# Optimization experiments

Measured on AMD Instinct MI355X. Metric: run time of the kernel, lower is better.

## Reference

```python
import jax, jax.numpy as jnp
import numpy as np


def _conv(x, w, b):
    # NCHW conv with 'same' padding derived from kernel size (matches nn.Conv2d padding=k//2)
    ph, pw = w.shape[2] // 2, w.shape[3] // 2
    y = jax.lax.conv_general_dilated(
        x, w, window_strides=(1, 1), padding=[(ph, ph), (pw, pw)],
        dimension_numbers=("NCHW", "OIHW", "NCHW"))
    return y + b[None, :, None, None]


def _attn(q, k, v):
    # q,k,v: [N,C,H,W]; spatial self-attention over S=H*W positions
    N, C, H, W = q.shape
    S = H * W
    qf = q.reshape(N, C, S)
    kf = k.reshape(N, C, S)
    vf = v.reshape(N, C, S)
    scores = jnp.einsum("ncs,nct->nst", qf, kf) / jnp.sqrt(jnp.asarray(C, qf.dtype))
    a = jax.nn.softmax(scores, axis=-1)
    z = jnp.einsum("nst,nct->ncs", a, vf)
    return z.reshape(N, C, H, W)


def setup_inputs() -> dict:
    key = jax.random.key(0)
    ks = jax.random.split(key, 14)
    B, T, Ci, Hd, H, W = 4, 10, 1, 64, 32, 32
    sc = 0.05
    return {
        "x": jax.random.uniform(ks[0], (B, T, Ci, H, W), jnp.float32),
        # SAConvLSTMCell main conv: (Ci+Hd) -> 4*Hd, 3x3
        "w_conv": jax.random.normal(ks[1], (4 * Hd, Ci + Hd, 3, 3), jnp.float32) * sc,
        "b_conv": jax.random.normal(ks[2], (4 * Hd,), jnp.float32) * sc,
        # SA conv_h: Hd -> 3*Hd, 1x1
        "w_h": jax.random.normal(ks[3], (3 * Hd, Hd, 1, 1), jnp.float32) * sc,
        "b_h": jax.random.normal(ks[4], (3 * Hd,), jnp.float32) * sc,
        # SA conv_m: Hd -> 2*Hd, 1x1
        "w_m": jax.random.normal(ks[5], (2 * Hd, Hd, 1, 1), jnp.float32) * sc,
        "b_m": jax.random.normal(ks[6], (2 * Hd,), jnp.float32) * sc,
        # SA conv_z: 2*Hd -> Hd, 1x1
        "w_z": jax.random.normal(ks[7], (Hd, 2 * Hd, 1, 1), jnp.float32) * sc,
        "b_z": jax.random.normal(ks[8], (Hd,), jnp.float32) * sc,
        # SA conv_output: 2*Hd -> 3*Hd, 3x3
        "w_sa": jax.random.normal(ks[9], (3 * Hd, 2 * Hd, 3, 3), jnp.float32) * sc,
        "b_sa": jax.random.normal(ks[10], (3 * Hd,), jnp.float32) * sc,
        # conv_out: Hd -> Ci, 1x1
        "w_co": jax.random.normal(ks[11], (Ci, Hd, 1, 1), jnp.float32) * sc,
        "b_co": jax.random.normal(ks[12], (Ci,), jnp.float32) * sc,
        "future_frames": 10,
    }


def reference(x, w_conv, b_conv, w_h, b_h, w_m, b_m, w_z, b_z,
              w_sa, b_sa, w_co, b_co, future_frames):
    B, T, Ci, H, W = x.shape
    Hd = w_conv.shape[0] // 4

    def cell(xt, h, c, m):
        cc = _conv(jnp.concatenate([xt, h], axis=1), w_conv, b_conv)
        i, f, o, g = jnp.split(cc, 4, axis=1)
        c_new = jax.nn.sigmoid(f) * c + jax.nn.sigmoid(i) * jnp.tanh(g)
        h_cur = jax.nn.sigmoid(o) * jnp.tanh(c_new)
        # spatial self-attention memory update
        hq, hk, hv = jnp.split(_conv(h_cur, w_h, b_h), 3, axis=1)
        mk, mv = jnp.split(_conv(m, w_m, b_m), 2, axis=1)
        Zh = _attn(hq, hk, hv)
        Zm = _attn(hq, mk, mv)
        Z = _conv(jnp.concatenate([Zh, Zm], axis=1), w_z, b_z)
        i2, g2, o2 = jnp.split(_conv(jnp.concatenate([Z, h_cur], axis=1), w_sa, b_sa), 3, axis=1)
        i2 = jax.nn.sigmoid(i2)
        m_new = i2 * jnp.tanh(g2) + (1.0 - i2) * m
        h_new = jax.nn.sigmoid(o2) * m_new
        return h_new, c_new, m_new

    z = jnp.zeros((B, Hd, H, W), x.dtype)
    state0 = (z, z, z)

    def enc_step(carry, xt):
        h, c, m = carry
        return cell(xt, h, c, m), None

    (h, c, m), _ = jax.lax.scan(enc_step, state0, jnp.moveaxis(x, 1, 0))

    # first decoder input: raw conv_out(h) (no sigmoid, per the original code path)
    inp0 = _conv(h, w_co, b_co)

    def dec_step(carry, _):
        h, c, m, inp = carry
        h, c, m = cell(inp, h, c, m)
        pred = jax.nn.sigmoid(_conv(h, w_co, b_co))
        return (h, c, m, pred), pred

    _, preds = jax.lax.scan(dec_step, (h, c, m, inp0), None, length=future_frames)
    return jnp.moveaxis(preds, 0, 1)  # [B, future_frames, Ci, H, W]
```

## Files before the change

kernel.cpp:

```cpp
#include <hip/hip_runtime.h>
#include <math.h>

#define SS 1024

typedef unsigned short u16;
typedef __attribute__((ext_vector_type(8))) __bf16 bf16x8;
typedef __attribute__((ext_vector_type(4))) float f32x4;

#define MFMA(a,b,c) __builtin_amdgcn_mfma_f32_16x16x32_bf16(a,b,c,0,0,0)

__device__ __forceinline__ float sigm(float x){ return 1.f/(1.f+__expf(-x)); }
__device__ __forceinline__ u16 f2b(float x){ return __builtin_bit_cast(u16,(__bf16)x); }
__device__ __forceinline__ float b2f(u16 u){ return (float)__builtin_bit_cast(__bf16,u); }
__device__ __forceinline__ bf16x8 ldb8(const u16* p){ return *(const bf16x8*)p; }
__device__ __forceinline__ void st4b(u16* p, const f32x4 v){
  union { u16 u[4]; uint2 w; } t;
  t.u[0]=f2b(v[0]); t.u[1]=f2b(v[1]); t.u[2]=f2b(v[2]); t.u[3]=f2b(v[3]);
  *(uint2*)p = t.w;
}

__global__ __launch_bounds__(256) void k_prep(
    const float* __restrict__ wconv, const float* __restrict__ wh,
    const float* __restrict__ wm, const float* __restrict__ wz,
    const float* __restrict__ wsa,
    u16* __restrict__ Wg, u16* __restrict__ Whm,
    u16* __restrict__ Wzp, u16* __restrict__ Wsap)
{
  const int idx = blockIdx.x*256 + threadIdx.x;
  if (idx < 155648) {
    const int step = idx >> 13, co = (idx >> 5) & 255, j = idx & 31;
    float v = 0.f;
    if (step < 18) {
      const int tap = step >> 1, ci = 1 + (step & 1)*32 + j;
      v = wconv[co*585 + ci*9 + tap];
    } else if (j < 9) {
      v = wconv[co*585 + j];
    }
    Wg[idx] = f2b(v);
    return;
  }
  int l = idx - 155648;
  if (l < 20480) {
    const int step = l / 10240, row = (l >> 5) % 320, j = l & 31;
    const int ci = step*32 + j;
    const float v = (row < 192) ? wh[row*64+ci]*(row < 64 ? 0.125f : 1.f)
                                : wm[(row-192)*64+ci];
    Whm[l] = f2b(v);
    return;
  }
  l -= 20480;
  if (l < 8192) {
    const int step = l >> 11, co = (l >> 5) & 63, j = l & 31;
    Wzp[l] = f2b(wz[co*128 + step*32 + j]);
    return;
  }
  l -= 8192;
  if (l < 221184) {
    const int step = l / 6144, co = (l >> 5) % 192, j = l & 31;
    const int tap = step >> 2, ci = (step & 3)*32 + j;
    Wsap[l] = f2b(wsa[(co*128+ci)*9 + tap]);
  }
}

__global__ __launch_bounds__(512) void k_A(
    const u16* __restrict__ hTb, const float* __restrict__ xsrc, int xbs,
    const u16* __restrict__ Wg, const float* __restrict__ bconv,
    float* __restrict__ cT, u16* __restrict__ xcat,
    const u16* __restrict__ mTb, const u16* __restrict__ Whm,
    const float* __restrict__ bh, const float* __restrict__ bm,
    u16* __restrict__ qT, u16* __restrict__ kT, u16* __restrict__ mkT,
    u16* __restrict__ vC, u16* __restrict__ mvC)
{
  __shared__ u16 hcl[16][72];
  __shared__ float part[4][4][64][4];
  const int b = blockIdx.y, s0 = blockIdx.x*16;
  const int tid = threadIdx.x, wid = tid>>6, lane = tid&63, gl = lane>>4, n = lane&15;
  const int ww = wid & 3, kh = wid >> 2;
  const u16* hb = hTb + (size_t)b*SS*64;
  const int s = s0 + n, y = s>>5, xx = s&31;
  f32x4 acc[4];
#pragma unroll
  for (int g4 = 0; g4 < 4; ++g4) {
    if (kh == 0) {
      const int co = g4*64 + ww*16 + gl*4;
      acc[g4] = (f32x4){ bconv[co], bconv[co+1], bconv[co+2], bconv[co+3] };
    } else {
      acc[g4] = (f32x4){0.f,0.f,0.f,0.f};
    }
  }
#pragma unroll
  for (int ss = 0; ss < 9; ++ss) {
    const int step = kh*9 + ss;
    const int tap = step>>1, half = step&1;
    const int dy = tap/3 - 1, dx = tap%3 - 1;
    const bool ok = ((unsigned)(y+dy) < 32u) & ((unsigned)(xx+dx) < 32u);
    const int sc = ok ? (s + dy*32 + dx) : s;
    bf16x8 bv = ldb8(hb + (size_t)sc*64 + half*32 + gl*8);
    bv = ok ? bv : (bf16x8){};
#pragma unroll
    for (int g4 = 0; g4 < 4; ++g4) {
      const bf16x8 a = ldb8(Wg + step*8192 + (g4*64 + ww*16 + n)*32 + gl*8);
      acc[g4] = MFMA(a, bv, acc[g4]);
    }
  }
  if (kh == 1) {
    bf16x8 xb;
    {
      union { u16 u[8]; bf16x8 v; } t;
#pragma unroll
      for (int jj = 0; jj < 8; ++jj) t.u[jj] = 0;
      if (gl == 0) {
#pragma unroll
        for (int jj = 0; jj < 8; ++jj) {
          const int dy = jj/3 - 1, dx = jj%3 - 1;
          if ((unsigned)(y+dy) < 32u && (unsigned)(xx+dx) < 32u)
            t.u[jj] = f2b(xsrc[b*xbs + s + dy*32 + dx]);
        }
      } else if (gl == 1) {
        if (y+1 < 32 && xx+1 < 32) t.u[0] = f2b(xsrc[b*xbs + s + 33]);
      }
      xb = t.v;
    }
#pragma unroll
    for (int g4 = 0; g4 < 4; ++g4) {
      const bf16x8 a = ldb8(Wg + 18*8192 + (g4*64 + ww*16 + n)*32 + gl*8);
      acc[g4] = MFMA(a, xb, acc[g4]);
    }
#pragma unroll
    for (int g4 = 0; g4 < 4; ++g4)
      *(f32x4*)&part[ww][g4][lane][0] = acc[g4];
  }
  __syncthreads();
  const int r0 = ww*16, cb = r0 + gl*4;
  if (kh == 0) {
#pragma unroll
    for (int g4 = 0; g4 < 4; ++g4) {
      const f32x4 p = *(const f32x4*)&part[ww][g4][lane][0];
      acc[g4][0]+=p[0]; acc[g4][1]+=p[1]; acc[g4][2]+=p[2]; acc[g4][3]+=p[3];
    }
    const int hd0 = cb;
    float* cp = cT + ((size_t)b*SS + s)*64 + hd0;
    f32x4 cv = *(f32x4*)cp, hcv;
#pragma unroll
    for (int rr = 0; rr < 4; ++rr) {
      const float cn = sigm(acc[1][rr])*cv[rr] + sigm(acc[0][rr])*tanhf(acc[3][rr]);
      cv[rr] = cn;
      hcv[rr] = sigm(acc[2][rr])*tanhf(cn);
    }
    *(f32x4*)cp = cv;
    st4b(xcat + ((size_t)b*SS + s)*128 + 64 + hd0, hcv);
    st4b(&hcl[n][hd0], hcv);
  } else {
    f32x4 a3 = (f32x4){ bm[cb], bm[cb+1], bm[cb+2], bm[cb+3] };
    f32x4 a4 = (f32x4){ bm[64+cb], bm[64+cb+1], bm[64+cb+2], bm[64+cb+3] };
#pragma unroll
    for (int step = 0; step < 2; ++step) {
      const bf16x8 bmm = ldb8(mTb + ((size_t)b*SS+s)*64 + step*32 + gl*8);
      a3 = MFMA(ldb8(Whm + step*10240 + (3*64 + r0 + n)*32 + gl*8), bmm, a3);
      a4 = MFMA(ldb8(Whm + step*10240 + (4*64 + r0 + n)*32 + gl*8), bmm, a4);
    }
    const size_t ps = ((size_t)b*SS + s)*64 + cb;
    st4b(mkT + ps, a3);
#pragma unroll
    for (int rr = 0; rr < 4; ++rr)
      mvC[((size_t)b*64 + cb + rr)*SS + s] = f2b(a4[rr]);
  }
  __syncthreads();
  if (kh == 0) {
    f32x4 a0 = (f32x4){ bh[cb]*0.125f, bh[cb+1]*0.125f, bh[cb+2]*0.125f, bh[cb+3]*0.125f };
    f32x4 a1 = (f32x4){ bh[64+cb], bh[64+cb+1], bh[64+cb+2], bh[64+cb+3] };
    f32x4 a2 = (f32x4){ bh[128+cb], bh[128+cb+1], bh[128+cb+2], bh[128+cb+3] };
#pragma unroll
    for (int step = 0; step < 2; ++step) {
      const bf16x8 bhc = ldb8(&hcl[n][step*32 + gl*8]);
      a0 = MFMA(ldb8(Whm + step*10240 + (0*64 + r0 + n)*32 + gl*8), bhc, a0);
      a1 = MFMA(ldb8(Whm + step*10240 + (1*64 + r0 + n)*32 + gl*8), bhc, a1);
      a2 = MFMA(ldb8(Whm + step*10240 + (2*64 + r0 + n)*32 + gl*8), bhc, a2);
    }
    const size_t ps = ((size_t)b*SS + s)*64 + cb;
    st4b(qT + ps, a0);
    st4b(kT + ps, a1);
#pragma unroll
    for (int rr = 0; rr < 4; ++rr)
      vC[((size_t)b*64 + cb + rr)*SS + s] = f2b(a2[rr]);
  }
}

__global__ __launch_bounds__(512) void k_B(
    const u16* __restrict__ qT, const u16* __restrict__ kT,
    const u16* __restrict__ mkT, const u16* __restrict__ vC,
    const u16* __restrict__ mvC,
    const u16* __restrict__ Wzp, const float* __restrict__ bz,
    u16* __restrict__ xcat)
{
  __shared__ u16 ldsP[8*16*72];
  __shared__ float oS[2][3][16][65];
  __shared__ float mS[2][3][16], lS[2][3][16];
  __shared__ u16 zbuf[16][136];
  const int tid = threadIdx.x, wid = tid>>6, lane = tid&63, gl = lane>>4, n = lane&15;
  const int b = blockIdx.y, s0 = blockIdx.x*16;
  const int at = wid & 1, kv = wid >> 1;
  const u16* qb = qT + (size_t)b*SS*64;
  const u16* kb = (at ? mkT : kT) + (size_t)b*SS*64;
  const u16* vb = (at ? mvC : vC) + (size_t)b*64*SS;
  const bf16x8 bq0 = ldb8(qb + (size_t)(s0+n)*64 + gl*8);
  const bf16x8 bq1 = ldb8(qb + (size_t)(s0+n)*64 + 32 + gl*8);
  f32x4 o[4];
#pragma unroll
  for (int ct = 0; ct < 4; ++ct) o[ct] = (f32x4){0.f,0.f,0.f,0.f};
  float mrun = -1e30f, lrun = 0.f;
  u16* pb = ldsP + wid*1152 + n*72;

#pragma unroll 1
  for (int step = 0; step < 4; ++step) {
    const int t0 = kv*256 + step*64;
    f32x4 st4[4];
#pragma unroll
    for (int tt = 0; tt < 4; ++tt) {
      const u16* kr = kb + (size_t)(t0 + tt*16 + n)*64;
      f32x4 a = {0.f,0.f,0.f,0.f};
      a = MFMA(ldb8(kr + gl*8), bq0, a);
      a = MFMA(ldb8(kr + 32 + gl*8), bq1, a);
      st4[tt] = a;
    }
    float mt = -1e30f;
#pragma unroll
    for (int tt = 0; tt < 4; ++tt)
#pragma unroll
      for (int rr = 0; rr < 4; ++rr) mt = fmaxf(mt, st4[tt][rr]);
    mt = fmaxf(mt, __shfl_xor(mt, 16));
    mt = fmaxf(mt, __shfl_xor(mt, 32));
    const float mnew = fmaxf(mrun, mt);
    const float f = __expf(mrun - mnew);
    float ps = 0.f;
#pragma unroll
    for (int tt = 0; tt < 4; ++tt) {
      const float p0e = __expf(st4[tt][0]-mnew), p1e = __expf(st4[tt][1]-mnew);
      const float p2e = __expf(st4[tt][2]-mnew), p3e = __expf(st4[tt][3]-mnew);
      ps += (p0e + p1e) + (p2e + p3e);
      *(unsigned*)(pb + tt*16 + gl*4)     = (unsigned)f2b(p0e) | ((unsigned)f2b(p1e)<<16);
      *(unsigned*)(pb + tt*16 + gl*4 + 2) = (unsigned)f2b(p2e) | ((unsigned)f2b(p3e)<<16);
    }
    ps += __shfl_xor(ps, 16);
    ps += __shfl_xor(ps, 32);
    lrun = lrun*f + ps;
    mrun = mnew;
    float fr[4];
#pragma unroll
    for (int rr = 0; rr < 4; ++rr) fr[rr] = __shfl(f, gl*4 + rr);
#pragma unroll
    for (int ct = 0; ct < 4; ++ct)
#pragma unroll
      for (int rr = 0; rr < 4; ++rr) o[ct][rr] *= fr[rr];
    const bf16x8 pa0 = ldb8(pb + gl*8);
    const bf16x8 pa1 = ldb8(pb + 32 + gl*8);
#pragma unroll
    for (int ct = 0; ct < 4; ++ct) {
      const u16* vr = vb + (size_t)(ct*16 + n)*SS + t0;
      o[ct] = MFMA(pa0, ldb8(vr + gl*8), o[ct]);
      o[ct] = MFMA(pa1, ldb8(vr + 32 + gl*8), o[ct]);
    }
  }
  if (kv > 0) {
#pragma unroll
    for (int ct = 0; ct < 4; ++ct)
#pragma unroll
      for (int rr = 0; rr < 4; ++rr) oS[at][kv-1][gl*4+rr][ct*16+n] = o[ct][rr];
    if (gl == 0) { mS[at][kv-1][n] = mrun; lS[at][kv-1][n] = lrun; }
  }
  __syncthreads();
  if (kv == 0) {
    const float m1 = mS[at][0][n], m2 = mS[at][1][n], m3 = mS[at][2][n];
    const float l1 = lS[at][0][n], l2 = lS[at][1][n], l3 = lS[at][2][n];
    const float mm = fmaxf(fmaxf(mrun, m1), fmaxf(m2, m3));
    const float e0 = __expf(mrun - mm), e1 = __expf(m1 - mm);
    const float e2 = __expf(m2 - mm),   e3 = __expf(m3 - mm);
    const float inv = 1.f / (lrun*e0 + l1*e1 + l2*e2 + l3*e3);
    const float a0 = e0*inv, a1v = e1*inv, a2v = e2*inv, a3v = e3*inv;
    float f0r[4], f1r[4], f2r[4], f3r[4];
#pragma unroll
    for (int rr = 0; rr < 4; ++rr) {
      f0r[rr] = __shfl(a0, gl*4 + rr);
      f1r[rr] = __shfl(a1v, gl*4 + rr);
      f2r[rr] = __shfl(a2v, gl*4 + rr);
      f3r[rr] = __shfl(a3v, gl*4 + rr);
    }
#pragma unroll
    for (int ct = 0; ct < 4; ++ct)
#pragma unroll
      for (int rr = 0; rr < 4; ++rr) {
        const int q = gl*4 + rr, c = ct*16 + n;
        zbuf[q][at*64 + c] = f2b(o[ct][rr]*f0r[rr] + oS[at][0][q][c]*f1r[rr]
                                 + oS[at][1][q][c]*f2r[rr] + oS[at][2][q][c]*f3r[rr]);
      }
  }
  __syncthreads();
  if (wid < 4) {
    const int co = wid*16 + gl*4;
    f32x4 acc = (f32x4){ bz[co], bz[co+1], bz[co+2], bz[co+3] };
#pragma unroll
    for (int qq = 0; qq < 4; ++qq) {
      const bf16x8 bv = ldb8(&zbuf[n][qq*32 + gl*8]);
      const bf16x8 a = ldb8(Wzp + qq*2048 + (wid*16 + n)*32 + gl*8);
      acc = MFMA(a, bv, acc);
    }
    st4b(xcat + ((size_t)b*SS + s0 + n)*128 + co, acc);
  }
}

__global__ __launch_bounds__(768) void k_C(
    const u16* __restrict__ xcat, const u16* __restrict__ Wsap,
    const float* __restrict__ bsa,
    float* __restrict__ mT, u16* __restrict__ mTb, u16* __restrict__ hTb,
    const float* __restrict__ wco, const float* __restrict__ bco,
    float* __restrict__ inp, float* __restrict__ out, int mode, int j)
{
  __shared__ float part[2][4][3][64][4];
  __shared__ float pool[16][17];
  const int b = blockIdx.y, s0 = blockIdx.x*16;
  const int tid = threadIdx.x, wid = tid>>6, lane = tid&63, gl = lane>>4, n = lane&15;
  const int whd = wid & 3, kq = wid >> 2;
  const int hd0 = whd*16 + gl*4;
  const int s = s0 + n, y = s>>5, xx = s&31;
  f32x4 acc[3];
#pragma unroll
  for (int i = 0; i < 3; ++i) {
    if (kq == 0) {
      const int co = i*64 + hd0;
      acc[i] = (f32x4){ bsa[co], bsa[co+1], bsa[co+2], bsa[co+3] };
    } else {
      acc[i] = (f32x4){0.f,0.f,0.f,0.f};
    }
  }
#pragma unroll
  for (int ss = 0; ss < 12; ++ss) {
    const int step = kq*12 + ss;
    const int tap = step>>2, qq = step&3;
    const int dy = tap/3 - 1, dx = tap%3 - 1;
    const bool ok = ((unsigned)(y+dy) < 32u) & ((unsigned)(xx+dx) < 32u);
    const int sc = ok ? (s + dy*32 + dx) : s;
    bf16x8 bv = ldb8(xcat + ((size_t)b*SS + sc)*128 + qq*32 + gl*8);
    bv = ok ? bv : (bf16x8){};
#pragma unroll
    for (int i = 0; i < 3; ++i) {
      const bf16x8 a = ldb8(Wsap + step*6144 + (i*64 + whd*16 + n)*32 + gl*8);
      acc[i] = MFMA(a, bv, acc[i]);
    }
  }
  if (kq > 0) {
#pragma unroll
    for (int i = 0; i < 3; ++i)
      *(f32x4*)&part[kq-1][whd][i][lane][0] = acc[i];
  }
  __syncthreads();
  if (kq == 0) {
#pragma unroll
    for (int i = 0; i < 3; ++i) {
      const f32x4 p0 = *(const f32x4*)&part[0][whd][i][lane][0];
      const f32x4 p1 = *(const f32x4*)&part[1][whd][i][lane][0];
      acc[i][0] += p0[0] + p1[0]; acc[i][1] += p0[1] + p1[1];
      acc[i][2] += p0[2] + p1[2]; acc[i][3] += p0[3] + p1[3];
    }
    float* mp = mT + ((size_t)b*SS + s)*64 + hd0;
    f32x4 mv4 = *(f32x4*)mp, hv;
#pragma unroll
    for (int rr = 0; rr < 4; ++rr) {
      const float i2 = sigm(acc[0][rr]);
      const float mn = i2*tanhf(acc[1][rr]) + (1.f - i2)*mv4[rr];
      mv4[rr] = mn;
      hv[rr] = sigm(acc[2][rr])*mn;
    }
    *(f32x4*)mp = mv4;
    st4b(mTb + ((size_t)b*SS + s)*64 + hd0, mv4);
    st4b(hTb + ((size_t)b*SS + s)*64 + hd0, hv);
    if (mode >= 0)
      pool[n][whd*4 + gl] = hv[0]*wco[hd0] + hv[1]*wco[hd0+1]
                          + hv[2]*wco[hd0+2] + hv[3]*wco[hd0+3];
  }
  if (mode >= 0) {
    __syncthreads();
    if (tid < 16) {
      float v = bco[0];
#pragma unroll
      for (int i = 0; i < 16; ++i) v += pool[tid][i];
      const int sp = s0 + tid;
      if (mode == 1) {
        v = sigm(v);
        out[((size_t)b*10 + j)*SS + sp] = v;
      }
      inp[b*SS + sp] = v;
    }
  }
}

extern "C" void kernel_launch(void* const* d_in, const int* in_sizes, int n_in,
                              void* d_out, int out_size, void* d_ws, size_t ws_size,
                              hipStream_t stream) {
  const float* x      = (const float*)d_in[0];
  const float* w_conv = (const float*)d_in[1];
  const float* b_conv = (const float*)d_in[2];
  const float* w_h    = (const float*)d_in[3];
  const float* b_h    = (const float*)d_in[4];
  const float* w_m    = (const float*)d_in[5];
  const float* b_m    = (const float*)d_in[6];
  const float* w_z    = (const float*)d_in[7];
  const float* b_z    = (const float*)d_in[8];
  const float* w_sa   = (const float*)d_in[9];
  const float* b_sa   = (const float*)d_in[10];
  const float* w_co   = (const float*)d_in[11];
  const float* b_co   = (const float*)d_in[12];
  float* out = (float*)d_out;

  float* ws  = (float*)d_ws;
  float* cT  = ws;
  float* mT  = ws + 262144;
  float* inp = ws + 524288;
  u16* ub   = (u16*)(ws + 528384);
  u16* hTb  = ub;
  u16* mTb  = ub + 262144;
  u16* xcat = ub + 524288;
  u16* qT   = ub + 1048576;
  u16* kT   = ub + 1310720;
  u16* mkT  = ub + 1572864;
  u16* vC   = ub + 1835008;
  u16* mvC  = ub + 2097152;
  u16* Wg   = ub + 2359296;
  u16* Whm  = ub + 2514944;
  u16* Wzp  = ub + 2535424;
  u16* Wsap = ub + 2543616;

  hipMemsetAsync(ws, 0, (size_t)524288*4, stream);
  hipMemsetAsync(hTb, 0, (size_t)524288*2, stream);
  k_prep<<<dim3(1584), 256, 0, stream>>>(w_conv, w_h, w_m, w_z, w_sa, Wg, Whm, Wzp, Wsap);

  auto cell = [&](const float* xsrc, int xbs, int mode, int j) {
    k_A<<<dim3(64,4), 512, 0, stream>>>(hTb, xsrc, xbs, Wg, b_conv, cT, xcat,
                                        mTb, Whm, b_h, b_m, qT, kT, mkT, vC, mvC);
    k_B<<<dim3(64,4), 512, 0, stream>>>(qT, kT, mkT, vC, mvC, Wzp, b_z, xcat);
    k_C<<<dim3(64,4), 768, 0, stream>>>(xcat, Wsap, b_sa, mT, mTb, hTb,
                                        w_co, b_co, inp, out, mode, j);
  };

  for (int t = 0; t < 10; ++t)
    cell(x + (size_t)t*SS, 10*SS, (t == 9) ? 0 : -1, 0);
  for (int j = 0; j < 10; ++j)
    cell(inp, SS, 1, j);
}
```

Baseline: 980.8 us.

## Fold state zeroing into prep kernel, stage x halo in LDS, double-buffer attention P

Drops the two memset launches and zeroes the c, m, h and m-bf16 state buffers inside the weight-prep kernel, which saves launch overhead. In k_A the 3x18 input halo is loaded once into shared memory, so the im2col gather of x reads LDS instead of issuing scattered global loads per lane; this adds one extra __syncthreads. In k_B the softmax P buffer is double-buffered across steps and the step loop is fully unrolled, aiming to remove a write-after-read hazard and allow overlap. In exchange k_B uses more shared memory, which may lower occupancy.

```diff
diff --git a/kernel.cpp b/kernel.cpp
--- a/kernel.cpp
+++ b/kernel.cpp
@@ -24,9 +24,14 @@
     const float* __restrict__ wm, const float* __restrict__ wz,
     const float* __restrict__ wsa,
     u16* __restrict__ Wg, u16* __restrict__ Whm,
-    u16* __restrict__ Wzp, u16* __restrict__ Wsap)
+    u16* __restrict__ Wzp, u16* __restrict__ Wsap,
+    float* __restrict__ cT, float* __restrict__ mT,
+    u16* __restrict__ hTb, u16* __restrict__ mTb)
 {
   const int idx = blockIdx.x*256 + threadIdx.x;
+  if (idx < 262144) {
+    cT[idx] = 0.f; mT[idx] = 0.f; hTb[idx] = 0; mTb[idx] = 0;
+  }
   if (idx < 155648) {
     const int step = idx >> 13, co = (idx >> 5) & 255, j = idx & 31;
     float v = 0.f;
@@ -73,11 +78,21 @@
 {
   __shared__ u16 hcl[16][72];
   __shared__ float part[4][4][64][4];
+  __shared__ float xtile[3][20];
   const int b = blockIdx.y, s0 = blockIdx.x*16;
   const int tid = threadIdx.x, wid = tid>>6, lane = tid&63, gl = lane>>4, n = lane&15;
   const int ww = wid & 3, kh = wid >> 2;
   const u16* hb = hTb + (size_t)b*SS*64;
   const int s = s0 + n, y = s>>5, xx = s&31;
+  if (tid < 60) {
+    const int r = tid/20, c = tid%20;
+    const int yy = (s0>>5) + r - 1, xc = (s0&31) + c - 1;
+    float v = 0.f;
+    if ((unsigned)yy < 32u && (unsigned)xc < 32u && c < 18)
+      v = xsrc[b*xbs + yy*32 + xc];
+    xtile[r][c] = v;
+  }
+  __syncthreads();
   f32x4 acc[4];
 #pragma unroll
   for (int g4 = 0; g4 < 4; ++g4) {
@@ -111,13 +126,10 @@
       for (int jj = 0; jj < 8; ++jj) t.u[jj] = 0;
       if (gl == 0) {
 #pragma unroll
-        for (int jj = 0; jj < 8; ++jj) {
-          const int dy = jj/3 - 1, dx = jj%3 - 1;
-          if ((unsigned)(y+dy) < 32u && (unsigned)(xx+dx) < 32u)
-            t.u[jj] = f2b(xsrc[b*xbs + s + dy*32 + dx]);
-        }
+        for (int jj = 0; jj < 8; ++jj)
+          t.u[jj] = f2b(xtile[jj/3][n + jj%3]);
       } else if (gl == 1) {
-        if (y+1 < 32 && xx+1 < 32) t.u[0] = f2b(xsrc[b*xbs + s + 33]);
+        t.u[0] = f2b(xtile[2][n + 2]);
       }
       xb = t.v;
     }
@@ -193,7 +205,7 @@
     const u16* __restrict__ Wzp, const float* __restrict__ bz,
     u16* __restrict__ xcat)
 {
-  __shared__ u16 ldsP[8*16*72];
+  __shared__ u16 ldsP[2*8*16*72];
   __shared__ float oS[2][3][16][65];
   __shared__ float mS[2][3][16], lS[2][3][16];
   __shared__ u16 zbuf[16][136];
@@ -209,11 +221,11 @@
 #pragma unroll
   for (int ct = 0; ct < 4; ++ct) o[ct] = (f32x4){0.f,0.f,0.f,0.f};
   float mrun = -1e30f, lrun = 0.f;
-  u16* pb = ldsP + wid*1152 + n*72;
-
-#pragma unroll 1
+
+#pragma unroll
   for (int step = 0; step < 4; ++step) {
     const int t0 = kv*256 + step*64;
+    u16* pb = ldsP + ((step & 1)*8 + wid)*1152 + n*72;
     f32x4 st4[4];
 #pragma unroll
     for (int tt = 0; tt < 4; ++tt) {
@@ -429,9 +441,8 @@
   u16* Wzp  = ub + 2535424;
   u16* Wsap = ub + 2543616;
 
-  hipMemsetAsync(ws, 0, (size_t)524288*4, stream);
-  hipMemsetAsync(hTb, 0, (size_t)524288*2, stream);
-  k_prep<<<dim3(1584), 256, 0, stream>>>(w_conv, w_h, w_m, w_z, w_sa, Wg, Whm, Wzp, Wsap);
+  k_prep<<<dim3(1584), 256, 0, stream>>>(w_conv, w_h, w_m, w_z, w_sa,
+                                         Wg, Whm, Wzp, Wsap, cT, mT, hTb, mTb);
 
   auto cell = [&](const float* xsrc, int xbs, int mode, int j) {
     k_A<<<dim3(64,4), 512, 0, stream>>>(hTb, xsrc, xbs, Wg, b_conv, cT, xcat,
```

Result: no change. 971.4 us (-1.0%).
